# Performance work log

Measured on AMD Instinct MI355X. Metric: run time of the kernel, lower is better.

The kernel has to match this reference:

```python
import jax, jax.numpy as jnp
import numpy as np


def avg_pool2(x):
    # 2x2 average pool, stride 2, NCHW
    b, c, h, w = x.shape
    return x.reshape(b, c, h // 2, 2, w // 2, 2).mean(axis=(3, 5))


def bisr_conv(x, W, mvk, mvb, beta):
    # ReDistribution: per-channel affine
    x = x * mvk + mvb
    # Spectral binary activation with tanh STE (forward value == sign(x))
    t = jnp.tanh(x * beta)
    xb = jax.lax.stop_gradient(jnp.sign(x)) - jax.lax.stop_gradient(t) + t
    # Binary weights: per-output-channel scale * sign(W), clipped-weight STE
    scale = jnp.mean(jnp.abs(W), axis=(1, 2, 3), keepdims=True)  # [O,1,1,1]
    bw_ng = jax.lax.stop_gradient(scale * jnp.sign(W))
    cw = jnp.clip(W, -1.0, 1.0)
    bw = bw_ng - jax.lax.stop_gradient(cw) + cw
    return jax.lax.conv_general_dilated(
        xb, bw, window_strides=(1, 1), padding=((1, 1), (1, 1)),
        dimension_numbers=('NCHW', 'OIHW', 'NCHW'))


def rprelu(x, pb0, alpha, pb1):
    x = x + pb0
    x = jnp.where(x >= 0, x, alpha * x)  # per-channel PReLU
    return x + pb1


def setup_inputs() -> dict:
    key = jax.random.key(0)
    B, C, H, W = 16, 128, 128, 128
    ks = jax.random.split(key, 3)
    x = jax.random.normal(ks[0], (B, C, H, W), dtype=jnp.float32)
    def branch_params(k):
        Wt = jax.random.normal(k, (C, C, 3, 3), dtype=jnp.float32) * 0.001
        return Wt
    zeros_c = jnp.zeros((1, C, 1, 1), jnp.float32)
    ones_c = jnp.ones((1, C, 1, 1), jnp.float32)
    alpha = jnp.full((1, C, 1, 1), 0.25, jnp.float32)
    return {
        'x': x,
        'W1': branch_params(ks[1]), 'mvk1': ones_c, 'mvb1': zeros_c,
        'beta1': jnp.ones((1,), jnp.float32), 'pb0_1': zeros_c,
        'alpha1': alpha, 'pb1_1': zeros_c,
        'W2': branch_params(ks[2]), 'mvk2': ones_c, 'mvb2': zeros_c,
        'beta2': jnp.ones((1,), jnp.float32), 'pb0_2': zeros_c,
        'alpha2': alpha, 'pb1_2': zeros_c,
    }


def reference(x, W1, mvk1, mvb1, beta1, pb0_1, alpha1, pb1_1,
              W2, mvk2, mvb2, beta2, pb0_2, alpha2, pb1_2):
    out = avg_pool2(x)  # [B, C, H/2, W/2]
    out1 = out + rprelu(bisr_conv(out, W1, mvk1, mvb1, beta1), pb0_1, alpha1, pb1_1)
    out2 = out + rprelu(bisr_conv(out, W2, mvk2, mvb2, beta2), pb0_2, alpha2, pb1_2)
    return jnp.concatenate([out1, out2], axis=1)  # [B, 2C, H/2, W/2]
```

## Files before the change

kernel.cpp:

```cpp
#include <hip/hip_runtime.h>
#include <stdint.h>

#define BATCH 16
#define CH    128
#define HIN   128
#define WIN   128
#define PH    64
#define PW    64

#define OFF_ABITS  16777216u
#define OFF_WBITS  18874368u
#define OFF_WSCALE 18911232u
#define OFF_WCORR  18912256u

typedef _Float16 half2v __attribute__((ext_vector_type(2)));

__global__ __launch_bounds__(256) void pool_pack(
    const float* __restrict__ x,
    const float* __restrict__ mvk1, const float* __restrict__ mvb1,
    const float* __restrict__ mvk2, const float* __restrict__ mvb2,
    _Float16* __restrict__ pooled, uint32_t* __restrict__ abits)
{
    __shared__ float kL[2][128], bL[2][128];
    __shared__ unsigned short sb[2][64][8];
    const int b  = blockIdx.y;
    const int ph = blockIdx.x;
    const int t  = threadIdx.x;

    {
        const int br = t >> 7, c = t & 127;
        kL[br][c] = (br ? mvk2 : mvk1)[c];
        bL[br][c] = (br ? mvb2 : mvb1)[c];
    }
    __syncthreads();

    const int k31 = t & 31;
    const int g   = t >> 5;
    const int pw2 = 2 * k31;
    const float* xq = x + (((size_t)b * CH) * HIN + 2 * ph) * WIN + 4 * k31;
    uint32_t m00 = 0, m01 = 0, m10 = 0, m11 = 0;
    #pragma unroll
    for (int u = 0; u < 16; ++u) {
        const int c = g * 16 + u;
        const float* xr = xq + (size_t)c * (HIN * WIN);
        const float4 r0 = *(const float4*)xr;
        const float4 r1 = *(const float4*)(xr + WIN);
        const float q0 = (r0.x + r0.y + r1.x + r1.y) * 0.25f;
        const float q1 = (r0.z + r0.w + r1.z + r1.w) * 0.25f;
        union { _Float16 h[2]; uint32_t w; } pk;
        pk.h[0] = (_Float16)q0;
        pk.h[1] = (_Float16)q1;
        *(uint32_t*)(pooled + ((size_t)(b * CH + c) * (PH * PW)) + ph * PW + pw2) = pk.w;
        const float k0 = kL[0][c], b0 = bL[0][c];
        const float k1 = kL[1][c], b1 = bL[1][c];
        m00 |= (uint32_t)(fmaf(q0, k0, b0) < 0.0f) << u;
        m01 |= (uint32_t)(fmaf(q1, k0, b0) < 0.0f) << u;
        m10 |= (uint32_t)(fmaf(q0, k1, b1) < 0.0f) << u;
        m11 |= (uint32_t)(fmaf(q1, k1, b1) < 0.0f) << u;
    }
    sb[0][pw2][g]     = (unsigned short)m00;
    sb[0][pw2 + 1][g] = (unsigned short)m01;
    sb[1][pw2][g]     = (unsigned short)m10;
    sb[1][pw2 + 1][g] = (unsigned short)m11;
    __syncthreads();

    {
        const int wp = t & 1;
        const int px = (t >> 1) & 63;
        const int br = t >> 7;
        const unsigned short* h = &sb[br][px][wp * 4];
        uint2 v;
        v.x = (uint32_t)h[0] | ((uint32_t)h[1] << 16);
        v.y = (uint32_t)h[2] | ((uint32_t)h[3] << 16);
        ((uint2*)abits)[((size_t)(br * BATCH + b) * (PH * PW) + ph * PW + px) * 2 + wp] = v;
    }
}

__global__ __launch_bounds__(64) void wprep(
    const float* __restrict__ W1, const float* __restrict__ W2,
    uint32_t* __restrict__ wbits, float* __restrict__ wscale,
    int* __restrict__ wcorr)
{
    __shared__ uint32_t swb[9][4];
    __shared__ int tpv[9];
    const int bo = blockIdx.x;
    const int branch = bo >> 7;
    const int o = bo & 127;
    const float* Wt = (branch ? W2 : W1) + (size_t)o * (CH * 9);
    const int t = threadIdx.x;

    float s = 0.f;
    for (int i = t; i < CH * 9; i += 64) s += fabsf(Wt[i]);
    #pragma unroll
    for (int off = 32; off >= 1; off >>= 1) s += __shfl_down(s, off);
    if (t == 0) wscale[bo] = s * (1.0f / (CH * 9));

    if (t < 36) {
        const int tap  = t >> 2;
        const int word = t & 3;
        uint32_t bits = 0;
        for (int j = 0; j < 32; ++j) {
            const float wv = Wt[(word * 32 + j) * 9 + tap];
            bits |= (wv < 0.0f ? 1u : 0u) << j;
        }
        wbits[(bo * 9 + tap) * 4 + word] = bits;
        swb[tap][word] = bits;
    }
    __syncthreads();
    if (t < 9)
        tpv[t] = 2 * (__popc(swb[t][0]) + __popc(swb[t][1]) +
                      __popc(swb[t][2]) + __popc(swb[t][3])) - 128;
    __syncthreads();
    if (t == 0) {
        int* wc = wcorr + bo * 8;
        wc[0] = tpv[0] + tpv[1] + tpv[2];
        wc[1] = tpv[6] + tpv[7] + tpv[8];
        wc[2] = tpv[0] + tpv[3] + tpv[6];
        wc[3] = tpv[2] + tpv[5] + tpv[8];
        wc[4] = tpv[0];
        wc[5] = tpv[2];
        wc[6] = tpv[6];
        wc[7] = tpv[8];
    }
}

__device__ __forceinline__ int bcnt_acc(uint32_t xv, int acc) {
    int d;
    asm("v_bcnt_u32_b32 %0, %1, %2" : "=v"(d) : "v"(xv), "v"(acc));
    return d;
}
__device__ __forceinline__ int xacc4(uint4 a, uint4 w, int acc) {
    acc = bcnt_acc(a.x ^ w.x, acc);
    acc = bcnt_acc(a.y ^ w.y, acc);
    acc = bcnt_acc(a.z ^ w.z, acc);
    acc = bcnt_acc(a.w ^ w.w, acc);
    return acc;
}

__global__ __launch_bounds__(256, 8) void bconv_main(
    const uint32_t* __restrict__ abits_, const uint32_t* __restrict__ wbits_,
    const float* __restrict__ wscale, const int* __restrict__ wcorr,
    const _Float16* __restrict__ pooledH,
    const float* __restrict__ pb0_1, const float* __restrict__ alpha1, const float* __restrict__ pb1_1,
    const float* __restrict__ pb0_2, const float* __restrict__ alpha2, const float* __restrict__ pb1_2,
    float* __restrict__ out)
{
    __shared__ uint4 ha[10][66];
    const int bid = blockIdx.x;
    const int og     = bid & 7;
    const int ty     = (bid >> 3) & 7;
    const int b      = (bid >> 6) & 15;
    const int branch = bid >> 10;
    const int t  = threadIdx.x;
    const int cp = t & 31;
    const int r  = t >> 5;
    const int gr = ty * 8 + r;

    const uint4* ab = (const uint4*)abits_ + (size_t)(branch * BATCH + b) * (PH * PW);
    for (int e = t; e < 660; e += 256) {
        const int rr = e / 66, cc = e % 66;
        const int hp = ty * 8 - 1 + rr, wp = cc - 1;
        uint4 v = make_uint4(0u, 0u, 0u, 0u);
        if (hp >= 0 && hp < PH && wp >= 0 && wp < PW) v = ab[hp * PW + wp];
        ha[rr][cc] = v;
    }
    __syncthreads();

    uint4 a[3][4];
    #pragma unroll
    for (int i = 0; i < 3; ++i)
        #pragma unroll
        for (int j = 0; j < 4; ++j)
            a[i][j] = ha[r + i][2 * cp + j];

    const bool fr0 = (gr == 0), fr2 = (gr == 63);
    const bool fc0 = (cp == 0), fc2 = (cp == 31);

    const uint4* wb  = (const uint4*)wbits_ + (size_t)branch * (128 * 9);
    const int*   wcb = wcorr + branch * (128 * 8);
    const float* wsv = wscale + branch * 128;
    const float* pb0 = branch ? pb0_2  : pb0_1;
    const float* alp = branch ? alpha2 : alpha1;
    const float* pb1 = branch ? pb1_2  : pb1_1;

    const _Float16* prow = pooledH + (size_t)(b * CH) * (PH * PW) + gr * PW + 2 * cp;
    float* orow = out + (size_t)(b * 2 * CH + branch * CH) * (PH * PW) + gr * PW + 2 * cp;

    const int o_beg = og * 16;
    for (int o = o_beg; o < o_beg + 16; ++o) {
        int pc0 = 0, pc1 = 0;
        #pragma unroll
        for (int dy = 0; dy < 3; ++dy) {
            const uint4 w0 = wb[o * 9 + dy * 3 + 0];
            const uint4 w1 = wb[o * 9 + dy * 3 + 1];
            const uint4 w2 = wb[o * 9 + dy * 3 + 2];
            pc0 = xacc4(a[dy][0], w0, pc0);
            pc1 = xacc4(a[dy][1], w0, pc1);
            pc0 = xacc4(a[dy][1], w1, pc0);
            pc1 = xacc4(a[dy][2], w1, pc1);
            pc0 = xacc4(a[dy][2], w2, pc0);
            pc1 = xacc4(a[dy][3], w2, pc1);
        }
        const int4 wcA = *(const int4*)(wcb + o * 8);
        const int4 wcB = *(const int4*)(wcb + o * 8 + 4);
        const int baser = (fr0 ? wcA.x : 0) + (fr2 ? wcA.y : 0);
        const int cc0e  = wcA.z - (fr0 ? wcB.x : 0) - (fr2 ? wcB.z : 0);
        const int cc2e  = wcA.w - (fr0 ? wcB.y : 0) - (fr2 ? wcB.w : 0);
        const int S0 = 1152 + baser + (fc0 ? cc0e : 0) - 2 * pc0;
        const int S1 = 1152 + baser + (fc2 ? cc2e : 0) - 2 * pc1;

        const float sc = wsv[o], b0v = pb0[o], av = alp[o], b1v = pb1[o];
        float y0 = sc * (float)S0 + b0v;
        float y1 = sc * (float)S1 + b0v;
        y0 = fmaxf(y0, 0.f) + av * fminf(y0, 0.f) + b1v;
        y1 = fmaxf(y1, 0.f) + av * fminf(y1, 0.f) + b1v;
        const half2v pv = *(const half2v*)(prow + (size_t)o * (PH * PW));
        float2 st;
        st.x = (float)pv.x + y0;
        st.y = (float)pv.y + y1;
        *(float2*)(orow + (size_t)o * (PH * PW)) = st;
    }
}

extern "C" void kernel_launch(void* const* d_in, const int* in_sizes, int n_in,
                              void* d_out, int out_size, void* d_ws, size_t ws_size,
                              hipStream_t stream)
{
    const float* x      = (const float*)d_in[0];
    const float* W1     = (const float*)d_in[1];
    const float* mvk1   = (const float*)d_in[2];
    const float* mvb1   = (const float*)d_in[3];
    const float* pb0_1  = (const float*)d_in[5];
    const float* alpha1 = (const float*)d_in[6];
    const float* pb1_1  = (const float*)d_in[7];
    const float* W2     = (const float*)d_in[8];
    const float* mvk2   = (const float*)d_in[9];
    const float* mvb2   = (const float*)d_in[10];
    const float* pb0_2  = (const float*)d_in[12];
    const float* alpha2 = (const float*)d_in[13];
    const float* pb1_2  = (const float*)d_in[14];
    float* out = (float*)d_out;

    char* ws = (char*)d_ws;
    _Float16* pooled = (_Float16*)ws;
    uint32_t* abits  = (uint32_t*)(ws + OFF_ABITS);
    uint32_t* wbits  = (uint32_t*)(ws + OFF_WBITS);
    float*    wscale = (float*)(ws + OFF_WSCALE);
    int*      wcorr  = (int*)(ws + OFF_WCORR);

    hipLaunchKernelGGL(wprep, dim3(256), dim3(64), 0, stream, W1, W2, wbits, wscale, wcorr);
    hipLaunchKernelGGL(pool_pack, dim3(64, 16), dim3(256), 0, stream,
                       x, mvk1, mvb1, mvk2, mvb2, pooled, abits);
    hipLaunchKernelGGL(bconv_main, dim3(2048), dim3(256), 0, stream,
                       abits, wbits, wscale, wcorr, pooled,
                       pb0_1, alpha1, pb1_1, pb0_2, alpha2, pb1_2, out);
}
```

Before: 289.8 us.

## Store padded activation bitplanes and drop LDS halo staging in binary conv

Activation bit-planes are now written into a zero-padded 66x66 layout. Extra blocks in the weight-prep kernel zero the border ring, so the conv kernel can load its 3x4 neighbourhood straight from global memory instead of staging a halo tile in shared memory and synchronising. The change also adds nontemporal loads of the input in pooling and nontemporal stores of the output, plus a partial unroll of the output-channel loop. Without LDS staging, each loaded value is fetched redundantly by neighbouring threads through the cache, and the workspace offsets move to make room for the padded layout.

After: 275.0 us. 5.1% less time.

```diff
diff --git a/kernel.cpp b/kernel.cpp
--- a/kernel.cpp
+++ b/kernel.cpp
@@ -7,13 +7,17 @@
 #define WIN   128
 #define PH    64
 #define PW    64
+#define PADW  66
+#define IMGS  (PADW * PADW)
 
 #define OFF_ABITS  16777216u
-#define OFF_WBITS  18874368u
-#define OFF_WSCALE 18911232u
-#define OFF_WCORR  18912256u
+#define OFF_WBITS  19007488u
+#define OFF_WSCALE 19044352u
+#define OFF_WCORR  19045376u
 
 typedef _Float16 half2v __attribute__((ext_vector_type(2)));
+typedef float    fvec4  __attribute__((ext_vector_type(4)));
+typedef float    fvec2  __attribute__((ext_vector_type(2)));
 
 __global__ __launch_bounds__(256) void pool_pack(
     const float* __restrict__ x,
@@ -43,8 +47,8 @@
     for (int u = 0; u < 16; ++u) {
         const int c = g * 16 + u;
         const float* xr = xq + (size_t)c * (HIN * WIN);
-        const float4 r0 = *(const float4*)xr;
-        const float4 r1 = *(const float4*)(xr + WIN);
+        const fvec4 r0 = __builtin_nontemporal_load((const fvec4*)xr);
+        const fvec4 r1 = __builtin_nontemporal_load((const fvec4*)(xr + WIN));
         const float q0 = (r0.x + r0.y + r1.x + r1.y) * 0.25f;
         const float q1 = (r0.z + r0.w + r1.z + r1.w) * 0.25f;
         union { _Float16 h[2]; uint32_t w; } pk;
@@ -72,22 +76,38 @@
         uint2 v;
         v.x = (uint32_t)h[0] | ((uint32_t)h[1] << 16);
         v.y = (uint32_t)h[2] | ((uint32_t)h[3] << 16);
-        ((uint2*)abits)[((size_t)(br * BATCH + b) * (PH * PW) + ph * PW + px) * 2 + wp] = v;
+        ((uint2*)abits)[((size_t)(br * BATCH + b) * IMGS + (ph + 1) * PADW + px + 1) * 2 + wp] = v;
     }
 }
 
 __global__ __launch_bounds__(64) void wprep(
     const float* __restrict__ W1, const float* __restrict__ W2,
     uint32_t* __restrict__ wbits, float* __restrict__ wscale,
-    int* __restrict__ wcorr)
-{
+    int* __restrict__ wcorr, uint32_t* __restrict__ abits)
+{
+    const int bid = blockIdx.x;
+    const int t = threadIdx.x;
+
+    if (bid >= 256) {
+        const int img  = (bid - 256) >> 1;
+        const int half = bid & 1;
+        uint4* base = (uint4*)abits + (size_t)img * IMGS;
+        const uint4 z = make_uint4(0u, 0u, 0u, 0u);
+        for (int e = t; e < 130; e += 64) {
+            int rr, cc;
+            if (half == 0) { if (e < 66) { rr = 0;  cc = e; } else { rr = e - 65; cc = 0; } }
+            else           { if (e < 66) { rr = 65; cc = e; } else { rr = e - 65; cc = 65; } }
+            base[rr * PADW + cc] = z;
+        }
+        return;
+    }
+
     __shared__ uint32_t swb[9][4];
     __shared__ int tpv[9];
-    const int bo = blockIdx.x;
+    const int bo = bid;
     const int branch = bo >> 7;
     const int o = bo & 127;
     const float* Wt = (branch ? W2 : W1) + (size_t)o * (CH * 9);
-    const int t = threadIdx.x;
 
     float s = 0.f;
     for (int i = t; i < CH * 9; i += 64) s += fabsf(Wt[i]);
@@ -145,7 +165,6 @@
     const float* __restrict__ pb0_2, const float* __restrict__ alpha2, const float* __restrict__ pb1_2,
     float* __restrict__ out)
 {
-    __shared__ uint4 ha[10][66];
     const int bid = blockIdx.x;
     const int og     = bid & 7;
     const int ty     = (bid >> 3) & 7;
@@ -156,22 +175,14 @@
     const int r  = t >> 5;
     const int gr = ty * 8 + r;
 
-    const uint4* ab = (const uint4*)abits_ + (size_t)(branch * BATCH + b) * (PH * PW);
-    for (int e = t; e < 660; e += 256) {
-        const int rr = e / 66, cc = e % 66;
-        const int hp = ty * 8 - 1 + rr, wp = cc - 1;
-        uint4 v = make_uint4(0u, 0u, 0u, 0u);
-        if (hp >= 0 && hp < PH && wp >= 0 && wp < PW) v = ab[hp * PW + wp];
-        ha[rr][cc] = v;
-    }
-    __syncthreads();
-
+    const uint4* ab = (const uint4*)abits_ + (size_t)(branch * BATCH + b) * IMGS
+                    + (size_t)gr * PADW + 2 * cp;
     uint4 a[3][4];
     #pragma unroll
     for (int i = 0; i < 3; ++i)
         #pragma unroll
         for (int j = 0; j < 4; ++j)
-            a[i][j] = ha[r + i][2 * cp + j];
+            a[i][j] = ab[i * PADW + j];
 
     const bool fr0 = (gr == 0), fr2 = (gr == 63);
     const bool fc0 = (cp == 0), fc2 = (cp == 31);
@@ -187,6 +198,7 @@
     float* orow = out + (size_t)(b * 2 * CH + branch * CH) * (PH * PW) + gr * PW + 2 * cp;
 
     const int o_beg = og * 16;
+    #pragma unroll 4
     for (int o = o_beg; o < o_beg + 16; ++o) {
         int pc0 = 0, pc1 = 0;
         #pragma unroll
@@ -215,10 +227,10 @@
         y0 = fmaxf(y0, 0.f) + av * fminf(y0, 0.f) + b1v;
         y1 = fmaxf(y1, 0.f) + av * fminf(y1, 0.f) + b1v;
         const half2v pv = *(const half2v*)(prow + (size_t)o * (PH * PW));
-        float2 st;
+        fvec2 st;
         st.x = (float)pv.x + y0;
         st.y = (float)pv.y + y1;
-        *(float2*)(orow + (size_t)o * (PH * PW)) = st;
+        __builtin_nontemporal_store(st, (fvec2*)(orow + (size_t)o * (PH * PW)));
     }
 }
 
@@ -248,7 +260,8 @@
     float*    wscale = (float*)(ws + OFF_WSCALE);
     int*      wcorr  = (int*)(ws + OFF_WCORR);
 
-    hipLaunchKernelGGL(wprep, dim3(256), dim3(64), 0, stream, W1, W2, wbits, wscale, wcorr);
+    hipLaunchKernelGGL(wprep, dim3(320), dim3(64), 0, stream,
+                       W1, W2, wbits, wscale, wcorr, abits);
     hipLaunchKernelGGL(pool_pack, dim3(64, 16), dim3(256), 0, stream,
                        x, mvk1, mvb1, mvk2, mvb2, pooled, abits);
     hipLaunchKernelGGL(bconv_main, dim3(2048), dim3(256), 0, stream,
```
